# Performance work log

Measured on AMD Instinct MI355X. Metric: run time of the kernel, lower is better.

## Reference

```python
import jax, jax.numpy as jnp
import numpy as np

REPLACE = 4
REMAIN = 32
EPS = 1e-12


def _l2norm(x, axis):
    return x / jnp.maximum(jnp.linalg.norm(x, axis=axis, keepdims=True), EPS)


def setup_inputs() -> dict:
    key = jax.random.key(0)
    ks = jax.random.split(key, 16)
    B, d = 4096, 64
    n_users, n_entities, n_items = 100000, 200000, 50000
    K, n_cans, n_rel = 64, 64, 100
    return {
        "users": jax.random.randint(ks[0], (B,), 0, n_users),
        "items": jax.random.randint(ks[1], (B,), 0, n_items),
        "kg_neighbors": jax.random.randint(ks[2], (n_items, K), 0, n_entities),
        "all_candidates": jax.random.randint(ks[3], (n_rel, n_cans), 0, n_entities),
        "neighbor_relations": jax.random.randint(ks[4], (n_items, K), 0, n_rel),
        "user_all_embeddings": jax.random.normal(ks[5], (n_users, d), jnp.float32),
        "entity_all_embeddings": jax.random.normal(ks[6], (n_entities, d), jnp.float32),
        "item_embeddings": jax.random.normal(ks[7], (B, d), jnp.float32),
        "ui_W": jax.random.normal(ks[8], (2 * d, d), jnp.float32) / np.sqrt(2 * d),
        "ui_b": jnp.zeros((d,), jnp.float32),
        "e1_W": jax.random.normal(ks[9], (d, d), jnp.float32) / np.sqrt(d),
        "e1_b": jnp.zeros((d,), jnp.float32),
        "e2_W": jax.random.normal(ks[10], (d, d), jnp.float32) / np.sqrt(d),
        "e2_b": jnp.zeros((d,), jnp.float32),
    }


def reference(users, items, kg_neighbors, all_candidates, neighbor_relations,
              user_all_embeddings, entity_all_embeddings, item_embeddings,
              ui_W, ui_b, e1_W, e1_b, e2_W, e2_b):
    B = users.shape[0]
    d = user_all_embeddings.shape[1]
    idx_dtype = kg_neighbors.dtype

    neighbors = kg_neighbors[items]                      # [B, K]
    users_e = user_all_embeddings[users]                 # [B, d]
    ui_e = _l2norm(jnp.concatenate([users_e, item_embeddings], axis=1) @ ui_W + ui_b, 1)  # [B, d]

    # Step 1: score neighbors, pick top replace_num
    ne = _l2norm(entity_all_embeddings[neighbors] @ e1_W + e1_b, 2)   # [B, K, d]
    scores1 = jnp.einsum('bd,bkd->bk', ui_e, ne)
    logits1 = jax.nn.softmax(scores1, axis=1)
    step1_prob, step1_idx = jax.lax.top_k(logits1, REPLACE)          # [B, R]
    replaced = jnp.take_along_axis(neighbors, step1_idx, axis=1)     # [B, R]
    sel_rel = jnp.take_along_axis(neighbor_relations[items], step1_idx, axis=1)
    cf_kg1 = kg_neighbors.at[items[:, None], step1_idx].set(
        jnp.zeros((B, REPLACE), idx_dtype))
    ap1 = jnp.log(jnp.mean(step1_prob, axis=1))                      # [B]

    # Step 2: candidate pruning + sampling
    cands = all_candidates[sel_rel]                                  # [B, R, C]
    cands_e = entity_all_embeddings[cands]                           # [B, R, C, d]
    scores2 = jnp.einsum('bd,brcd->brc', users_e, cands_e)
    _, remain_idx = jax.lax.top_k(scores2, REMAIN)                   # [B, R, M]
    cands = jnp.take_along_axis(cands, remain_idx, axis=2).reshape(B * REPLACE, REMAIN)

    replaced_e = _l2norm(entity_all_embeddings[replaced] @ e1_W + e1_b, 2)
    replaced_e = replaced_e.reshape(B * REPLACE, d)
    cands_e2 = _l2norm(entity_all_embeddings[cands] @ e2_W + e2_b, 2)  # [BR, M, d]
    ui_rep = jnp.repeat(ui_e, REPLACE, axis=0)                         # [BR, d]
    s2 = jnp.einsum('nd,nmd->nm', ui_rep * replaced_e, cands_e2)       # [BR, M]
    logp2 = jax.nn.log_softmax(s2, axis=1)

    skey = jax.random.key(42)
    step2_idx = jax.random.categorical(skey, logp2, axis=1)           # [BR]
    rows = jnp.arange(B * REPLACE)
    step2_prob = jnp.exp(logp2[rows, step2_idx]).reshape(B, REPLACE)
    sel_ent = cands[rows, step2_idx].reshape(B, REPLACE)
    cf_kg2 = kg_neighbors.at[items[:, None], step1_idx].set(sel_ent.astype(idx_dtype))
    ap2 = jnp.log(jnp.mean(step1_prob, axis=1)) + jnp.log(jnp.mean(step2_prob, axis=1))
    return (cf_kg1, ap1, cf_kg2, ap2)
```

## Files before the change

kernel.cpp:

```cpp
#include <hip/hip_runtime.h>
#include <stdint.h>

#define EPS_NORM 1e-12f
#define F32_TINY 1.17549435e-38f

static __device__ __forceinline__ int rfl(int v) {
  return __builtin_amdgcn_readfirstlane(v);
}

__device__ __forceinline__ void threefry2x32(uint32_t k0, uint32_t k1,
                                             uint32_t x0, uint32_t x1,
                                             uint32_t& o0, uint32_t& o1) {
  uint32_t ks2 = k0 ^ k1 ^ 0x1BD11BDAu;
  x0 += k0; x1 += k1;
#define TF_ROT(r) { x0 += x1; x1 = (x1 << (r)) | (x1 >> (32 - (r))); x1 ^= x0; }
  TF_ROT(13) TF_ROT(15) TF_ROT(26) TF_ROT(6)
  x0 += k1; x1 += ks2 + 1u;
  TF_ROT(17) TF_ROT(29) TF_ROT(16) TF_ROT(24)
  x0 += ks2; x1 += k0 + 2u;
  TF_ROT(13) TF_ROT(15) TF_ROT(26) TF_ROT(6)
  x0 += k0; x1 += k1 + 3u;
  TF_ROT(17) TF_ROT(29) TF_ROT(16) TF_ROT(24)
  x0 += k1; x1 += ks2 + 4u;
  TF_ROT(13) TF_ROT(15) TF_ROT(26) TF_ROT(6)
  x0 += ks2; x1 += k0 + 5u;
#undef TF_ROT
  o0 = x0; o1 = x1;
}

#define PERM_IDX(p) ((((p) & 7) << 3) | ((p) >> 3))

__global__ __launch_bounds__(256, 4) void k_phase1(
    const float* __restrict__ E, const int* __restrict__ allc,
    const float* __restrict__ W1, const float* __restrict__ b1,
    const float* __restrict__ W2, const float* __restrict__ b2,
    const float* __restrict__ U, const int* __restrict__ users,
    const float* __restrict__ Iemb, const float* __restrict__ uiW,
    const float* __restrict__ uib, const int* __restrict__ kg,
    float* __restrict__ T1, float* __restrict__ T2c, float* __restrict__ Eg,
    float* __restrict__ uiE, float* __restrict__ out0, int* __restrict__ wkg2) {
  __shared__ float SM[8192];
  const int blk = blockIdx.x, tid = threadIdx.x;
  const int wv = tid >> 6, lane = tid & 63;
  const int NT1B = 782, NT2B = 25, NUIB = 256;
  if (blk < NT1B + NT2B) {
    const bool isT1 = blk < NT1B;
    {
      const float* W = isT1 ? W1 : W2;
      for (int idx = tid; idx < 4096; idx += 256) {
        int k = idx >> 6, c = idx & 63;
        SM[k * 64 + ((c & 7) * 8 + (c >> 3))] = W[idx];
      }
    }
    __syncthreads();
    const int rg = lane >> 3, cg = lane & 7;
    const int sub = lane >> 5, r = lane & 31;
    const float* bias = isT1 ? b1 : b2;
    float bv[8];
#pragma unroll
    for (int ci = 0; ci < 8; ++ci) bv[ci] = bias[ci * 8 + cg];
    float* eTw = SM + 4096 + wv * 1024;
    const float4* eT4 = reinterpret_cast<const float4*>(eTw);
    const float4* W4 = reinterpret_cast<const float4*>(SM);
#pragma unroll 1
    for (int t = 0; t < 2; ++t) {
      int batch = (isT1 ? blk : blk - NT1B) * 2 + t;
      int rbase = batch * 128 + wv * 32;
      if (isT1 && rbase >= 200000) continue;
      int srow = isT1 ? (rbase + r) : allc[rbase + r];
      const float4* Er = reinterpret_cast<const float4*>(E + (size_t)srow * 64);
      float y[4][8];
#pragma unroll
      for (int ri = 0; ri < 4; ++ri)
#pragma unroll
        for (int ci = 0; ci < 8; ++ci) y[ri][ci] = 0.f;
#pragma unroll 1
      for (int h = 0; h < 2; ++h) {
        float4 a0 = Er[h * 8 + sub * 4 + 0];
        float4 a1 = Er[h * 8 + sub * 4 + 1];
        float4 a2 = Er[h * 8 + sub * 4 + 2];
        float4 a3 = Er[h * 8 + sub * 4 + 3];
        float ev[16] = {a0.x, a0.y, a0.z, a0.w, a1.x, a1.y, a1.z, a1.w,
                        a2.x, a2.y, a2.z, a2.w, a3.x, a3.y, a3.z, a3.w};
#pragma unroll
        for (int kk = 0; kk < 16; ++kk)
          eTw[(sub * 16 + kk) * 32 + r] = ev[kk];
        if (!isT1) {
          float4* G = reinterpret_cast<float4*>(
              Eg + (size_t)(rbase + r) * 64 + h * 32 + sub * 16);
          G[0] = a0; G[1] = a1; G[2] = a2; G[3] = a3;
        }
#pragma unroll 8
        for (int kk = 0; kk < 32; ++kk) {
          float4 e4 = eT4[kk * 8 + rg];
          float4 wa = W4[(h * 32 + kk) * 16 + cg * 2];
          float4 wb = W4[(h * 32 + kk) * 16 + cg * 2 + 1];
          float ev4[4] = {e4.x, e4.y, e4.z, e4.w};
          float wv8[8] = {wa.x, wa.y, wa.z, wa.w, wb.x, wb.y, wb.z, wb.w};
#pragma unroll
          for (int ri = 0; ri < 4; ++ri)
#pragma unroll
            for (int ci = 0; ci < 8; ++ci)
              y[ri][ci] = fmaf(ev4[ri], wv8[ci], y[ri][ci]);
        }
      }
#pragma unroll
      for (int ri = 0; ri < 4; ++ri)
#pragma unroll
        for (int ci = 0; ci < 8; ++ci)
          y[ri][ci] = __fadd_rn(y[ri][ci], bv[ci]);
#pragma unroll
      for (int ri = 0; ri < 4; ++ri) {
        float A0 = __fadd_rn(__fmul_rn(y[ri][0], y[ri][0]),
                             __fmul_rn(y[ri][4], y[ri][4]));
        float A1 = __fadd_rn(__fmul_rn(y[ri][1], y[ri][1]),
                             __fmul_rn(y[ri][5], y[ri][5]));
        float A2 = __fadd_rn(__fmul_rn(y[ri][2], y[ri][2]),
                             __fmul_rn(y[ri][6], y[ri][6]));
        float A3 = __fadd_rn(__fmul_rn(y[ri][3], y[ri][3]),
                             __fmul_rn(y[ri][7], y[ri][7]));
        float B0 = __fadd_rn(A0, A2), B1 = __fadd_rn(A1, A3);
        float C = __fadd_rn(B0, B1);
        C = __fadd_rn(C, __shfl_xor(C, 4));
        C = __fadd_rn(C, __shfl_xor(C, 2));
        C = __fadd_rn(C, __shfl_xor(C, 1));
        float denom = fmaxf(sqrtf(C), EPS_NORM);
        int row = rbase + rg * 4 + ri;
        if (isT1) {
          float4* drow = reinterpret_cast<float4*>(T1 + (size_t)row * 64 + cg * 8);
          drow[0] = make_float4(y[ri][0] / denom, y[ri][1] / denom,
                                y[ri][2] / denom, y[ri][3] / denom);
          drow[1] = make_float4(y[ri][4] / denom, y[ri][5] / denom,
                                y[ri][6] / denom, y[ri][7] / denom);
        } else {
          float* drow = T2c + (size_t)row * 64;
#pragma unroll
          for (int ci = 0; ci < 8; ++ci) drow[ci * 8 + cg] = y[ri][ci] / denom;
        }
      }
    }
  } else if (blk < NT1B + NT2B + NUIB) {
    int ub = blk - (NT1B + NT2B);
    for (int i = tid; i < 8192; i += 256) SM[i] = uiW[i];
    __syncthreads();
    float bl = uib[lane];
#pragma unroll 1
    for (int t = 0; t < 4; ++t) {
      int b = ub * 16 + wv * 4 + t;
      int usr = rfl(users[b]);
      const float* ur = U + (size_t)usr * 64;
      const float* ir = Iemb + (size_t)b * 64;
      float y = 0.f;
#pragma unroll
      for (int k = 0; k < 64; ++k) y = fmaf(ur[k], SM[k * 64 + lane], y);
#pragma unroll
      for (int k = 0; k < 64; ++k) y = fmaf(ir[k], SM[(64 + k) * 64 + lane], y);
      y += bl;
      float ss = y * y;
#pragma unroll
      for (int off = 32; off; off >>= 1) ss += __shfl_xor(ss, off);
      float yn = y / fmaxf(sqrtf(ss), EPS_NORM);
      uiE[(size_t)b * 64 + lane] = yn;
    }
  } else {
    const int4* kg4 = reinterpret_cast<const int4*>(kg);
    float4* o4 = reinterpret_cast<float4*>(out0);
    int4* w4 = reinterpret_cast<int4*>(wkg2);
    for (int i = (blk - 1063) * 256 + tid; i < 800000; i += 200 * 256) {
      int4 v = kg4[i];
      o4[i] = make_float4((float)v.x, (float)v.y, (float)v.z, (float)v.w);
      w4[i] = v;
    }
  }
}

__global__ __launch_bounds__(256) void k_init(const int* __restrict__ kg,
                                              float* __restrict__ out0,
                                              int* __restrict__ wkg2, int n) {
  int i = blockIdx.x * 256 + threadIdx.x;
  if (i < n) { int v = kg[i]; out0[i] = (float)v; wkg2[i] = v; }
}

__device__ __forceinline__ void transform_row(const float4* __restrict__ Er,
                                              const float* __restrict__ W,
                                              const float* __restrict__ bias,
                                              float (&yn)[64]) {
  float y[64];
#pragma unroll
  for (int j = 0; j < 64; ++j) y[j] = 0.f;
  float4 c0 = Er[0], c1 = Er[1], c2 = Er[2], c3 = Er[3];
#pragma unroll 1
  for (int cc = 0; cc < 4; ++cc) {
    float4 n0, n1, n2, n3;
    if (cc < 3) { n0 = Er[cc * 4 + 4]; n1 = Er[cc * 4 + 5];
                  n2 = Er[cc * 4 + 6]; n3 = Er[cc * 4 + 7]; }
    float ev[16] = {c0.x, c0.y, c0.z, c0.w, c1.x, c1.y, c1.z, c1.w,
                    c2.x, c2.y, c2.z, c2.w, c3.x, c3.y, c3.z, c3.w};
#pragma unroll
    for (int k2i = 0; k2i < 16; ++k2i) {
      const float4* Wr = reinterpret_cast<const float4*>(
          W + ((size_t)(cc * 16 + k2i)) * 64);
      float ek = ev[k2i];
#pragma unroll
      for (int j4 = 0; j4 < 16; ++j4) {
        float4 w = Wr[j4];
        y[j4 * 4 + 0] = fmaf(ek, w.x, y[j4 * 4 + 0]);
        y[j4 * 4 + 1] = fmaf(ek, w.y, y[j4 * 4 + 1]);
        y[j4 * 4 + 2] = fmaf(ek, w.z, y[j4 * 4 + 2]);
        y[j4 * 4 + 3] = fmaf(ek, w.w, y[j4 * 4 + 3]);
      }
    }
    c0 = n0; c1 = n1; c2 = n2; c3 = n3;
  }
  const float4* B4 = reinterpret_cast<const float4*>(bias);
#pragma unroll
  for (int j4 = 0; j4 < 16; ++j4) {
    float4 bb = B4[j4];
    float bv[4] = {bb.x, bb.y, bb.z, bb.w};
#pragma unroll
    for (int t = 0; t < 4; ++t) y[j4 * 4 + t] = __fadd_rn(y[j4 * 4 + t], bv[t]);
  }
  float S1[32];
#pragma unroll
  for (int i = 0; i < 32; ++i)
    S1[i] = __fadd_rn(__fmul_rn(y[i], y[i]), __fmul_rn(y[i + 32], y[i + 32]));
#pragma unroll
  for (int i = 0; i < 16; ++i) S1[i] = __fadd_rn(S1[i], S1[i + 16]);
#pragma unroll
  for (int i = 0; i < 8; ++i)  S1[i] = __fadd_rn(S1[i], S1[i + 8]);
#pragma unroll
  for (int i = 0; i < 4; ++i)  S1[i] = __fadd_rn(S1[i], S1[i + 4]);
#pragma unroll
  for (int i = 0; i < 2; ++i)  S1[i] = __fadd_rn(S1[i], S1[i + 2]);
  float ss = __fadd_rn(S1[0], S1[1]);
  float denom = fmaxf(sqrtf(ss), EPS_NORM);
#pragma unroll
  for (int j = 0; j < 64; ++j) yn[j] = y[j] / denom;
}

__global__ __launch_bounds__(256) void k_transform64(
    const float* __restrict__ src, const int* __restrict__ gidx,
    const float* __restrict__ W, const float* __restrict__ bias,
    float* __restrict__ out, int nrows) {
  __shared__ float Wl[4096];
  for (int i = threadIdx.x; i < 4096; i += 256) Wl[i] = W[i];
  __syncthreads();
  int wid = threadIdx.x >> 6, lane = threadIdx.x & 63;
  int row = rfl(blockIdx.x * 4 + wid);
  if (row >= nrows) return;
  int srow = rfl(gidx ? gidx[row] : row);
  const float* er = src + (size_t)srow * 64;
  float y = 0.f;
#pragma unroll
  for (int k = 0; k < 64; ++k) y = fmaf(er[k], Wl[k * 64 + lane], y);
  y += bias[lane];
  float ss = y * y;
#pragma unroll
  for (int off = 32; off; off >>= 1) ss += __shfl_xor(ss, off);
  float yn = y / fmaxf(sqrtf(ss), EPS_NORM);
  out[(size_t)row * 64 + lane] = yn;
}

__global__ __launch_bounds__(256) void k_ui(
    const float* __restrict__ U, const int* __restrict__ users,
    const float* __restrict__ Iemb, const float* __restrict__ W,
    const float* __restrict__ bias, float* __restrict__ out, int B) {
  __shared__ float Wl[8192];
  for (int i = threadIdx.x; i < 8192; i += 256) Wl[i] = W[i];
  __syncthreads();
  int wid = threadIdx.x >> 6, lane = threadIdx.x & 63;
  int b = rfl(blockIdx.x * 4 + wid);
  if (b >= B) return;
  int usr = rfl(users[b]);
  const float* ur = U + (size_t)usr * 64;
  const float* ir = Iemb + (size_t)b * 64;
  float y = 0.f;
#pragma unroll
  for (int k = 0; k < 64; ++k) y = fmaf(ur[k], Wl[k * 64 + lane], y);
#pragma unroll
  for (int k = 0; k < 64; ++k) y = fmaf(ir[k], Wl[(64 + k) * 64 + lane], y);
  y += bias[lane];
  float ss = y * y;
#pragma unroll
  for (int off = 32; off; off >>= 1) ss += __shfl_xor(ss, off);
  float yn = y / fmaxf(sqrtf(ss), EPS_NORM);
  out[(size_t)b * 64 + lane] = yn;
}

__device__ __forceinline__ void score1_tail(
    float s, int lane, int b, int item, int nb,
    const int* __restrict__ nrel,
    float* __restrict__ out0, float* __restrict__ ap1_out,
    int* __restrict__ s1_idx, int* __restrict__ s1_rel, int* __restrict__ s1_ent,
    float* __restrict__ lmp1) {
  float m = s;
#pragma unroll
  for (int off = 32; off; off >>= 1) m = fmaxf(m, __shfl_xor(m, off));
  float ex = expf(s - m);
  float sum = ex;
#pragma unroll
  for (int off = 32; off; off >>= 1) sum += __shfl_xor(sum, off);
  float p = ex / sum;
  int rank = 0;
  for (int k2 = 0; k2 < 64; ++k2) {
    float pv = __shfl(p, k2);
    rank += (pv > p || (pv == p && k2 < lane)) ? 1 : 0;
  }
  float acc = 0.f;
#pragma unroll
  for (int rr = 0; rr < 4; ++rr) {
    unsigned long long msk = __ballot(rank == rr);
    int src = __ffsll(msk) - 1;
    acc += __shfl(p, src);
  }
  float lm = logf(acc * 0.25f);
  if (lane == 0) { ap1_out[b] = lm; lmp1[b] = lm; }
  if (rank < 4) {
    s1_idx[b * 4 + rank] = lane;
    s1_ent[b * 4 + rank] = nb;
    s1_rel[b * 4 + rank] = nrel[(size_t)item * 64 + lane];
    out0[(size_t)item * 64 + lane] = 0.0f;
  }
}

__global__ __launch_bounds__(256) void k_score1g(
    const int* __restrict__ items, const int* __restrict__ kg,
    const int* __restrict__ nrel, const float* __restrict__ T1,
    const float* __restrict__ uiE,
    float* __restrict__ out0, float* __restrict__ ap1_out,
    int* __restrict__ s1_idx, int* __restrict__ s1_rel, int* __restrict__ s1_ent,
    float* __restrict__ lmp1) {
  int tid = threadIdx.x, wv = tid >> 6, lane = tid & 63;
  int b = rfl(blockIdx.x * 4 + wv);
  int item = rfl(items[b]);
  int nb = kg[(size_t)item * 64 + lane];
  const float4* R = reinterpret_cast<const float4*>(T1 + (size_t)nb * 64);
  float yn[64];
#pragma unroll
  for (int p4 = 0; p4 < 16; ++p4) {
    float4 v = R[p4];
    yn[PERM_IDX(4 * p4 + 0)] = v.x;
    yn[PERM_IDX(4 * p4 + 1)] = v.y;
    yn[PERM_IDX(4 * p4 + 2)] = v.z;
    yn[PERM_IDX(4 * p4 + 3)] = v.w;
  }
  const float4* Ur = reinterpret_cast<const float4*>(uiE + (size_t)b * 64);
  float D[32];
#pragma unroll
  for (int i4 = 0; i4 < 8; ++i4) {
    float4 ua = Ur[i4], ub = Ur[i4 + 8];
    float uav[4] = {ua.x, ua.y, ua.z, ua.w};
    float ubv[4] = {ub.x, ub.y, ub.z, ub.w};
#pragma unroll
    for (int t = 0; t < 4; ++t) {
      int i = i4 * 4 + t;
      D[i] = __fadd_rn(__fmul_rn(yn[i], uav[t]), __fmul_rn(yn[i + 32], ubv[t]));
    }
  }
#pragma unroll
  for (int i = 0; i < 16; ++i) D[i] = __fadd_rn(D[i], D[i + 16]);
#pragma unroll
  for (int i = 0; i < 8; ++i)  D[i] = __fadd_rn(D[i], D[i + 8]);
#pragma unroll
  for (int i = 0; i < 4; ++i)  D[i] = __fadd_rn(D[i], D[i + 4]);
#pragma unroll
  for (int i = 0; i < 2; ++i)  D[i] = __fadd_rn(D[i], D[i + 2]);
  float s = __fadd_rn(D[0], D[1]);
  score1_tail(s, lane, b, item, nb, nrel, out0, ap1_out, s1_idx, s1_rel, s1_ent, lmp1);
}

__global__ __launch_bounds__(256) void k_score1(
    const int* __restrict__ items, const int* __restrict__ kg,
    const int* __restrict__ nrel, const float* __restrict__ E,
    const float* __restrict__ W1, const float* __restrict__ b1,
    const float* __restrict__ uiE,
    float* __restrict__ out0, float* __restrict__ ap1_out,
    int* __restrict__ s1_idx, int* __restrict__ s1_rel, int* __restrict__ s1_ent,
    float* __restrict__ lmp1) {
  int tid = threadIdx.x, wv = tid >> 6, lane = tid & 63;
  int b = rfl(blockIdx.x * 4 + wv);
  int item = rfl(items[b]);
  int nb = kg[(size_t)item * 64 + lane];
  const float4* Er = reinterpret_cast<const float4*>(E + (size_t)nb * 64);
  float yn[64];
  transform_row(Er, W1, b1, yn);
  const float4* Ur = reinterpret_cast<const float4*>(uiE + (size_t)b * 64);
  float D[32];
#pragma unroll
  for (int i4 = 0; i4 < 8; ++i4) {
    float4 ua = Ur[i4], ub = Ur[i4 + 8];
    float uav[4] = {ua.x, ua.y, ua.z, ua.w};
    float ubv[4] = {ub.x, ub.y, ub.z, ub.w};
#pragma unroll
    for (int t = 0; t < 4; ++t) {
      int i = i4 * 4 + t;
      D[i] = __fadd_rn(__fmul_rn(yn[i], uav[t]), __fmul_rn(yn[i + 32], ubv[t]));
    }
  }
#pragma unroll
  for (int i = 0; i < 16; ++i) D[i] = __fadd_rn(D[i], D[i + 16]);
#pragma unroll
  for (int i = 0; i < 8; ++i)  D[i] = __fadd_rn(D[i], D[i + 8]);
#pragma unroll
  for (int i = 0; i < 4; ++i)  D[i] = __fadd_rn(D[i], D[i + 4]);
#pragma unroll
  for (int i = 0; i < 2; ++i)  D[i] = __fadd_rn(D[i], D[i + 2]);
  float s = __fadd_rn(D[0], D[1]);
  score1_tail(s, lane, b, item, nb, nrel, out0, ap1_out, s1_idx, s1_rel, s1_ent, lmp1);
}

__global__ __launch_bounds__(256) void k_score2e(
    const int* __restrict__ users, const int* __restrict__ s1_rel,
    const float* __restrict__ U, const float* __restrict__ Eg,
    const int* __restrict__ allc, int* __restrict__ kept, int N) {
  int wid = threadIdx.x >> 6, lane = threadIdx.x & 63;
  int n = rfl(blockIdx.x * 4 + wid);
  if (n >= N) return;
  int b = n >> 2;
  int rel = rfl(s1_rel[n]);
  int usr = rfl(users[b]);
  int ent = allc[rel * 64 + lane];
  const float* ur = U + (size_t)usr * 64;
  const float4* e4 = reinterpret_cast<const float4*>(Eg + ((size_t)rel * 64 + lane) * 64);
  float s = 0.f;
#pragma unroll
  for (int j4 = 0; j4 < 16; ++j4) {
    float4 t = e4[j4];
    s = fmaf(ur[4 * j4 + 0], t.x, s);
    s = fmaf(ur[4 * j4 + 1], t.y, s);
    s = fmaf(ur[4 * j4 + 2], t.z, s);
    s = fmaf(ur[4 * j4 + 3], t.w, s);
  }
  int rank = 0;
  for (int k2 = 0; k2 < 64; ++k2) {
    float sv = __shfl(s, k2);
    rank += (sv > s || (sv == s && k2 < lane)) ? 1 : 0;
  }
  if (rank < 32) kept[n * 32 + rank] = (lane << 18) | ent;
}

__global__ __launch_bounds__(256) void k_score2(
    const int* __restrict__ users, const int* __restrict__ s1_rel,
    const float* __restrict__ U, const float* __restrict__ E,
    const int* __restrict__ allc, int* __restrict__ kept, int N) {
  int wid = threadIdx.x >> 6, lane = threadIdx.x & 63;
  int n = rfl(blockIdx.x * 4 + wid);
  if (n >= N) return;
  int b = n >> 2;
  int rel = rfl(s1_rel[n]);
  int usr = rfl(users[b]);
  int ent = allc[rel * 64 + lane];
  const float* ur = U + (size_t)usr * 64;
  const float4* e4 = reinterpret_cast<const float4*>(E + (size_t)ent * 64);
  float s = 0.f;
#pragma unroll
  for (int j4 = 0; j4 < 16; ++j4) {
    float4 t = e4[j4];
    s = fmaf(ur[4 * j4 + 0], t.x, s);
    s = fmaf(ur[4 * j4 + 1], t.y, s);
    s = fmaf(ur[4 * j4 + 2], t.z, s);
    s = fmaf(ur[4 * j4 + 3], t.w, s);
  }
  int rank = 0;
  for (int k2 = 0; k2 < 64; ++k2) {
    float sv = __shfl(s, k2);
    rank += (sv > s || (sv == s && k2 < lane)) ? 1 : 0;
  }
  if (rank < 32) kept[n * 32 + rank] = (lane << 18) | ent;
}

template <bool PERMQ>
__device__ __forceinline__ void sample_body(
    float q, int n, int b, int lane,
    const int* __restrict__ items, const int* __restrict__ s1_idx,
    int rel, const float* __restrict__ T2c, const int* __restrict__ kept,
    float* __restrict__ p2, int* __restrict__ wkg2) {
  int m = lane & 31;
  int pk = kept[n * 32 + m];
  int c = pk >> 18;
  int ent = pk & 0x3FFFF;
  const float4* c4 = reinterpret_cast<const float4*>(T2c + ((size_t)rel * 64 + c) * 64);
  float s = 0.f;
#pragma unroll
  for (int j4 = 0; j4 < 16; ++j4) {
    float4 t = c4[j4];
    s = fmaf(__shfl(q, PERMQ ? PERM_IDX(4 * j4 + 0) : (4 * j4 + 0)), t.x, s);
    s = fmaf(__shfl(q, PERMQ ? PERM_IDX(4 * j4 + 1) : (4 * j4 + 1)), t.y, s);
    s = fmaf(__shfl(q, PERMQ ? PERM_IDX(4 * j4 + 2) : (4 * j4 + 2)), t.z, s);
    s = fmaf(__shfl(q, PERMQ ? PERM_IDX(4 * j4 + 3) : (4 * j4 + 3)), t.w, s);
  }
  float mx = s;
#pragma unroll
  for (int off = 1; off < 32; off <<= 1) mx = fmaxf(mx, __shfl_xor(mx, off));
  float shv = s - mx;
  float se = expf(shv);
  float sum = se;
#pragma unroll
  for (int off = 1; off < 32; off <<= 1) sum += __shfl_xor(sum, off);
  float logp = shv - logf(sum);
  uint32_t h0, h1;
  threefry2x32(0u, 42u, 0u, (uint32_t)(n * 32 + m), h0, h1);
  uint32_t bits = h0 ^ h1;
  float u0 = __uint_as_float((bits >> 9) | 0x3F800000u) - 1.0f;
  float uu = fmaxf(u0, F32_TINY);
  float g = -logf(-logf(uu));
  float z = g + logp;
  float bz = z; int bm = m;
#pragma unroll
  for (int off = 1; off < 32; off <<= 1) {
    float oz = __shfl_xor(bz, off);
    int om = __shfl_xor(bm, off);
    if (oz > bz || (oz == bz && om < bm)) { bz = oz; bm = om; }
  }
  if (lane == bm) {
    p2[n] = expf(logp);
    int col = s1_idx[n];
    int item = items[b];
    atomicMax(&wkg2[(size_t)item * 64 + col], ((b + 1) << 18) | ent);
  }
}

__global__ __launch_bounds__(256) void k_sample2(
    const int* __restrict__ items,
    const int* __restrict__ s1_idx, const int* __restrict__ s1_rel,
    const int* __restrict__ s1_ent, const float* __restrict__ T1,
    const float* __restrict__ T2c, const float* __restrict__ uiE,
    const int* __restrict__ kept,
    float* __restrict__ p2, int* __restrict__ wkg2, int N) {
  int tid = threadIdx.x, wid = tid >> 6, lane = tid & 63;
  int n = rfl(blockIdx.x * 4 + wid);
  if (n >= N) return;
  int b = n >> 2;
  int rel = rfl(s1_rel[n]);
  int repl = rfl(s1_ent[n]);
  int pl = PERM_IDX(lane);
  float q = uiE[(size_t)b * 64 + pl] * T1[(size_t)repl * 64 + lane];
  sample_body<true>(q, n, b, lane, items, s1_idx, rel, T2c, kept, p2, wkg2);
}

__global__ __launch_bounds__(256) void k_sample(
    const int* __restrict__ items,
    const int* __restrict__ s1_idx, const int* __restrict__ s1_rel,
    const int* __restrict__ s1_ent,
    const float* __restrict__ E, const float* __restrict__ W1,
    const float* __restrict__ b1, const float* __restrict__ T2c,
    const float* __restrict__ uiE, const int* __restrict__ kept,
    float* __restrict__ p2, int* __restrict__ wkg2, int N) {
  __shared__ float Wl[4096];
  int tid = threadIdx.x;
  for (int i = tid; i < 4096; i += 256) Wl[i] = W1[i];
  __syncthreads();
  int wid = tid >> 6, lane = tid & 63;
  int n = rfl(blockIdx.x * 4 + wid);
  if (n >= N) return;
  int b = n >> 2;
  int rel = rfl(s1_rel[n]);
  int repl = rfl(s1_ent[n]);
  const float* er = E + (size_t)repl * 64;
  float y = 0.f;
#pragma unroll
  for (int k2 = 0; k2 < 64; ++k2) y = fmaf(er[k2], Wl[k2 * 64 + lane], y);
  y += b1[lane];
  float ss = y * y;
#pragma unroll
  for (int off = 32; off; off >>= 1) ss += __shfl_xor(ss, off);
  float yn = y / fmaxf(sqrtf(ss), EPS_NORM);
  float q = uiE[(size_t)b * 64 + lane] * yn;
  sample_body<false>(q, n, b, lane, items, s1_idx, rel, T2c, kept, p2, wkg2);
}

__global__ __launch_bounds__(256) void k_fin(const int* __restrict__ wkg2,
                                             const float* __restrict__ p2,
                                             const float* __restrict__ lmp1,
                                             float* __restrict__ out2,
                                             float* __restrict__ out3,
                                             int n, int B) {
  int i = blockIdx.x * 256 + threadIdx.x;
  if (i < n) out2[i] = (float)(wkg2[i] & 0x3FFFF);
  if (i < B) {
    float a = ((p2[i * 4] + p2[i * 4 + 1]) + p2[i * 4 + 2]) + p2[i * 4 + 3];
    out3[i] = lmp1[i] + logf(a * 0.25f);
  }
}

extern "C" void kernel_launch(void* const* d_in, const int* in_sizes, int n_in,
                              void* d_out, int out_size, void* d_ws, size_t ws_size,
                              hipStream_t stream) {
  const int*   users = (const int*)d_in[0];
  const int*   items = (const int*)d_in[1];
  const int*   kg    = (const int*)d_in[2];
  const int*   allc  = (const int*)d_in[3];
  const int*   nrel  = (const int*)d_in[4];
  const float* U     = (const float*)d_in[5];
  const float* E     = (const float*)d_in[6];
  const float* Iemb  = (const float*)d_in[7];
  const float* uiW   = (const float*)d_in[8];
  const float* uib   = (const float*)d_in[9];
  const float* e1W   = (const float*)d_in[10];
  const float* e1b   = (const float*)d_in[11];
  const float* e2W   = (const float*)d_in[12];
  const float* e2b   = (const float*)d_in[13];

  const int B = 4096, NCELL = 3200000, NCAND = 6400, NR4 = 16384, NENT = 200000;

  float* out0    = (float*)d_out;
  float* out_ap1 = out0 + NCELL;
  float* out2    = out_ap1 + B;
  float* out_ap2 = out2 + NCELL;

  float* T2c  = (float*)d_ws;
  float* uiE  = T2c + 409600;
  int*   wkg2 = (int*)(uiE + 262144);
  int*   s1i  = wkg2 + NCELL;
  int*   s1r  = s1i + NR4;
  int*   s1e  = s1r + NR4;
  int*   kept = s1e + NR4;
  float* p2   = (float*)(kept + 524288);
  float* lmp1 = p2 + NR4;
  float* T1   = lmp1 + B;
  float* Eg   = out2;
  const size_t WS_NEED = ((size_t)(T1 + (size_t)NENT * 64) - (size_t)d_ws);
  const bool pathA = ws_size >= WS_NEED;

  if (pathA) {
    k_phase1<<<1263, 256, 0, stream>>>(E, allc, e1W, e1b, e2W, e2b, U, users,
                                       Iemb, uiW, uib, kg, T1, T2c, Eg, uiE,
                                       out0, wkg2);
    k_score1g<<<B / 4, 256, 0, stream>>>(items, kg, nrel, T1, uiE,
                                         out0, out_ap1, s1i, s1r, s1e, lmp1);
    k_score2e<<<(NR4 + 3) / 4, 256, 0, stream>>>(users, s1r, U, Eg, allc, kept, NR4);
    k_sample2<<<(NR4 + 3) / 4, 256, 0, stream>>>(items, s1i, s1r, s1e, T1, T2c,
                                                 uiE, kept, p2, wkg2, NR4);
  } else {
    k_init<<<(NCELL + 255) / 256, 256, 0, stream>>>(kg, out0, wkg2, NCELL);
    k_ui<<<(B + 3) / 4, 256, 0, stream>>>(U, users, Iemb, uiW, uib, uiE, B);
    k_transform64<<<(NCAND + 3) / 4, 256, 0, stream>>>(E, allc, e2W, e2b, T2c, NCAND);
    k_score1<<<B / 4, 256, 0, stream>>>(items, kg, nrel, E, e1W, e1b, uiE,
                                        out0, out_ap1, s1i, s1r, s1e, lmp1);
    k_score2<<<(NR4 + 3) / 4, 256, 0, stream>>>(users, s1r, U, E, allc, kept, NR4);
    k_sample<<<(NR4 + 3) / 4, 256, 0, stream>>>(items, s1i, s1r, s1e, E, e1W, e1b,
                                                T2c, uiE, kept, p2, wkg2, NR4);
  }
  k_fin<<<(NCELL + 255) / 256, 256, 0, stream>>>(wkg2, p2, lmp1, out2, out_ap2,
                                                 NCELL, B);
}
```

Baseline: 151.3 us.

## Write second output directly in phase1 and patch only replaced cells

In the main path, phase1 now writes the float copy of the KG table straight into the second output instead of staging an int copy in workspace. A new small finalize kernel converts only the 4 replaced cells per row from the work buffer. This removes the full-table pass that read and rewrote the whole 3.2M-cell table. The Eg staging copy of candidate embeddings is also dropped: score2 gathers from the entity table again, and phase1 loses its occupancy hint. Correctness now relies on score1 zeroing the work-buffer cells that the sampling kernel later fills.

Result: faster. 142.0 us (-6.2%).

```diff
diff --git a/kernel.cpp b/kernel.cpp
--- a/kernel.cpp
+++ b/kernel.cpp
@@ -30,15 +30,15 @@
 
 #define PERM_IDX(p) ((((p) & 7) << 3) | ((p) >> 3))
 
-__global__ __launch_bounds__(256, 4) void k_phase1(
+__global__ __launch_bounds__(256) void k_phase1(
     const float* __restrict__ E, const int* __restrict__ allc,
     const float* __restrict__ W1, const float* __restrict__ b1,
     const float* __restrict__ W2, const float* __restrict__ b2,
     const float* __restrict__ U, const int* __restrict__ users,
     const float* __restrict__ Iemb, const float* __restrict__ uiW,
     const float* __restrict__ uib, const int* __restrict__ kg,
-    float* __restrict__ T1, float* __restrict__ T2c, float* __restrict__ Eg,
-    float* __restrict__ uiE, float* __restrict__ out0, int* __restrict__ wkg2) {
+    float* __restrict__ T1, float* __restrict__ T2c,
+    float* __restrict__ uiE, float* __restrict__ out0, float* __restrict__ out2) {
   __shared__ float SM[8192];
   const int blk = blockIdx.x, tid = threadIdx.x;
   const int wv = tid >> 6, lane = tid & 63;
@@ -85,11 +85,6 @@
 #pragma unroll
         for (int kk = 0; kk < 16; ++kk)
           eTw[(sub * 16 + kk) * 32 + r] = ev[kk];
-        if (!isT1) {
-          float4* G = reinterpret_cast<float4*>(
-              Eg + (size_t)(rbase + r) * 64 + h * 32 + sub * 16);
-          G[0] = a0; G[1] = a1; G[2] = a2; G[3] = a3;
-        }
 #pragma unroll 8
         for (int kk = 0; kk < 32; ++kk) {
           float4 e4 = eT4[kk * 8 + rg];
@@ -165,11 +160,12 @@
   } else {
     const int4* kg4 = reinterpret_cast<const int4*>(kg);
     float4* o4 = reinterpret_cast<float4*>(out0);
-    int4* w4 = reinterpret_cast<int4*>(wkg2);
+    float4* o24 = reinterpret_cast<float4*>(out2);
     for (int i = (blk - 1063) * 256 + tid; i < 800000; i += 200 * 256) {
       int4 v = kg4[i];
-      o4[i] = make_float4((float)v.x, (float)v.y, (float)v.z, (float)v.w);
-      w4[i] = v;
+      float4 f = make_float4((float)v.x, (float)v.y, (float)v.z, (float)v.w);
+      o4[i] = f;
+      o24[i] = f;
     }
   }
 }
@@ -292,7 +288,7 @@
     const int* __restrict__ nrel,
     float* __restrict__ out0, float* __restrict__ ap1_out,
     int* __restrict__ s1_idx, int* __restrict__ s1_rel, int* __restrict__ s1_ent,
-    float* __restrict__ lmp1) {
+    float* __restrict__ lmp1, int* __restrict__ wkg2) {
   float m = s;
 #pragma unroll
   for (int off = 32; off; off >>= 1) m = fmaxf(m, __shfl_xor(m, off));
@@ -320,6 +316,7 @@
     s1_ent[b * 4 + rank] = nb;
     s1_rel[b * 4 + rank] = nrel[(size_t)item * 64 + lane];
     out0[(size_t)item * 64 + lane] = 0.0f;
+    wkg2[(size_t)item * 64 + lane] = 0;
   }
 }
 
@@ -329,7 +326,7 @@
     const float* __restrict__ uiE,
     float* __restrict__ out0, float* __restrict__ ap1_out,
     int* __restrict__ s1_idx, int* __restrict__ s1_rel, int* __restrict__ s1_ent,
-    float* __restrict__ lmp1) {
+    float* __restrict__ lmp1, int* __restrict__ wkg2) {
   int tid = threadIdx.x, wv = tid >> 6, lane = tid & 63;
   int b = rfl(blockIdx.x * 4 + wv);
   int item = rfl(items[b]);
@@ -366,7 +363,8 @@
 #pragma unroll
   for (int i = 0; i < 2; ++i)  D[i] = __fadd_rn(D[i], D[i + 2]);
   float s = __fadd_rn(D[0], D[1]);
-  score1_tail(s, lane, b, item, nb, nrel, out0, ap1_out, s1_idx, s1_rel, s1_ent, lmp1);
+  score1_tail(s, lane, b, item, nb, nrel, out0, ap1_out, s1_idx, s1_rel, s1_ent,
+              lmp1, wkg2);
 }
 
 __global__ __launch_bounds__(256) void k_score1(
@@ -376,7 +374,7 @@
     const float* __restrict__ uiE,
     float* __restrict__ out0, float* __restrict__ ap1_out,
     int* __restrict__ s1_idx, int* __restrict__ s1_rel, int* __restrict__ s1_ent,
-    float* __restrict__ lmp1) {
+    float* __restrict__ lmp1, int* __restrict__ wkg2) {
   int tid = threadIdx.x, wv = tid >> 6, lane = tid & 63;
   int b = rfl(blockIdx.x * 4 + wv);
   int item = rfl(items[b]);
@@ -406,37 +404,8 @@
 #pragma unroll
   for (int i = 0; i < 2; ++i)  D[i] = __fadd_rn(D[i], D[i + 2]);
   float s = __fadd_rn(D[0], D[1]);
-  score1_tail(s, lane, b, item, nb, nrel, out0, ap1_out, s1_idx, s1_rel, s1_ent, lmp1);
-}
-
-__global__ __launch_bounds__(256) void k_score2e(
-    const int* __restrict__ users, const int* __restrict__ s1_rel,
-    const float* __restrict__ U, const float* __restrict__ Eg,
-    const int* __restrict__ allc, int* __restrict__ kept, int N) {
-  int wid = threadIdx.x >> 6, lane = threadIdx.x & 63;
-  int n = rfl(blockIdx.x * 4 + wid);
-  if (n >= N) return;
-  int b = n >> 2;
-  int rel = rfl(s1_rel[n]);
-  int usr = rfl(users[b]);
-  int ent = allc[rel * 64 + lane];
-  const float* ur = U + (size_t)usr * 64;
-  const float4* e4 = reinterpret_cast<const float4*>(Eg + ((size_t)rel * 64 + lane) * 64);
-  float s = 0.f;
-#pragma unroll
-  for (int j4 = 0; j4 < 16; ++j4) {
-    float4 t = e4[j4];
-    s = fmaf(ur[4 * j4 + 0], t.x, s);
-    s = fmaf(ur[4 * j4 + 1], t.y, s);
-    s = fmaf(ur[4 * j4 + 2], t.z, s);
-    s = fmaf(ur[4 * j4 + 3], t.w, s);
-  }
-  int rank = 0;
-  for (int k2 = 0; k2 < 64; ++k2) {
-    float sv = __shfl(s, k2);
-    rank += (sv > s || (sv == s && k2 < lane)) ? 1 : 0;
-  }
-  if (rank < 32) kept[n * 32 + rank] = (lane << 18) | ent;
+  score1_tail(s, lane, b, item, nb, nrel, out0, ap1_out, s1_idx, s1_rel, s1_ent,
+              lmp1, wkg2);
 }
 
 __global__ __launch_bounds__(256) void k_score2(
@@ -569,6 +538,25 @@
   sample_body<false>(q, n, b, lane, items, s1_idx, rel, T2c, kept, p2, wkg2);
 }
 
+__global__ __launch_bounds__(256) void k_fin2(
+    const int* __restrict__ items, const int* __restrict__ s1_idx,
+    const int* __restrict__ wkg2, const float* __restrict__ p2,
+    const float* __restrict__ lmp1,
+    float* __restrict__ out2, float* __restrict__ out3, int N, int B) {
+  int i = blockIdx.x * 256 + threadIdx.x;
+  if (i < N) {
+    int b = i >> 2;
+    int item = items[b];
+    int col = s1_idx[i];
+    int v = wkg2[(size_t)item * 64 + col];
+    out2[(size_t)item * 64 + col] = (float)(v & 0x3FFFF);
+  }
+  if (i < B) {
+    float a = ((p2[i * 4] + p2[i * 4 + 1]) + p2[i * 4 + 2]) + p2[i * 4 + 3];
+    out3[i] = lmp1[i] + logf(a * 0.25f);
+  }
+}
+
 __global__ __launch_bounds__(256) void k_fin(const int* __restrict__ wkg2,
                                              const float* __restrict__ p2,
                                              const float* __restrict__ lmp1,
@@ -618,29 +606,30 @@
   float* p2   = (float*)(kept + 524288);
   float* lmp1 = p2 + NR4;
   float* T1   = lmp1 + B;
-  float* Eg   = out2;
   const size_t WS_NEED = ((size_t)(T1 + (size_t)NENT * 64) - (size_t)d_ws);
   const bool pathA = ws_size >= WS_NEED;
 
   if (pathA) {
     k_phase1<<<1263, 256, 0, stream>>>(E, allc, e1W, e1b, e2W, e2b, U, users,
-                                       Iemb, uiW, uib, kg, T1, T2c, Eg, uiE,
-                                       out0, wkg2);
+                                       Iemb, uiW, uib, kg, T1, T2c, uiE,
+                                       out0, out2);
     k_score1g<<<B / 4, 256, 0, stream>>>(items, kg, nrel, T1, uiE,
-                                         out0, out_ap1, s1i, s1r, s1e, lmp1);
-    k_score2e<<<(NR4 + 3) / 4, 256, 0, stream>>>(users, s1r, U, Eg, allc, kept, NR4);
+                                         out0, out_ap1, s1i, s1r, s1e, lmp1, wkg2);
+    k_score2<<<(NR4 + 3) / 4, 256, 0, stream>>>(users, s1r, U, E, allc, kept, NR4);
     k_sample2<<<(NR4 + 3) / 4, 256, 0, stream>>>(items, s1i, s1r, s1e, T1, T2c,
                                                  uiE, kept, p2, wkg2, NR4);
+    k_fin2<<<(NR4 + 255) / 256, 256, 0, stream>>>(items, s1i, wkg2, p2, lmp1,
+                                                  out2, out_ap2, NR4, B);
   } else {
     k_init<<<(NCELL + 255) / 256, 256, 0, stream>>>(kg, out0, wkg2, NCELL);
     k_ui<<<(B + 3) / 4, 256, 0, stream>>>(U, users, Iemb, uiW, uib, uiE, B);
     k_transform64<<<(NCAND + 3) / 4, 256, 0, stream>>>(E, allc, e2W, e2b, T2c, NCAND);
     k_score1<<<B / 4, 256, 0, stream>>>(items, kg, nrel, E, e1W, e1b, uiE,
-                                        out0, out_ap1, s1i, s1r, s1e, lmp1);
+                                        out0, out_ap1, s1i, s1r, s1e, lmp1, wkg2);
     k_score2<<<(NR4 + 3) / 4, 256, 0, stream>>>(users, s1r, U, E, allc, kept, NR4);
     k_sample<<<(NR4 + 3) / 4, 256, 0, stream>>>(items, s1i, s1r, s1e, E, e1W, e1b,
                                                 T2c, uiE, kept, p2, wkg2, NR4);
-  }
-  k_fin<<<(NCELL + 255) / 256, 256, 0, stream>>>(wkg2, p2, lmp1, out2, out_ap2,
-                                                 NCELL, B);
-}
+    k_fin<<<(NCELL + 255) / 256, 256, 0, stream>>>(wkg2, p2, lmp1, out2, out_ap2,
+                                                   NCELL, B);
+  }
+}
```
